# Kernel tuning notes

Measured on AMD Instinct MI355X. Metric: run time of the kernel, lower is better.

## Reference

```python
import jax, jax.numpy as jnp
import numpy as np

N = 10000
DIM = 64
F_CONST = 1.0
B_CONST = 0.1
R_CONST = 0.01


def setup_inputs() -> dict:
    key = jax.random.key(0)
    k1, k2 = jax.random.split(key)
    t = jnp.zeros((1,), dtype=jnp.float32)  # autonomous system; t unused
    x = jax.random.uniform(k1, (N, DIM), dtype=jnp.float32)
    A = jax.random.uniform(k2, (N, N), dtype=jnp.float32)
    return {"t": t, "x": x, "A": A}


def reference(t, x, A):
    # dx/dt = f - b*x - diag(A @ (r * x x^T)).reshape(-1, 1)
    # diag(A @ x x^T)_i = sum_j A_ij <x_j, x_i> = <x_i, (A @ x)_i>
    # so the interaction term is r * rowsum(x * (A @ x)) -- same math, no NxN intermediate.
    Ax = A @ x                                        # [N, DIM]
    outer = R_CONST * jnp.sum(x * Ax, axis=1, keepdims=True)  # [N, 1]
    return F_CONST - B_CONST * x - outer              # [N, DIM] via broadcast
```

## Files before the change

### kernel.cpp

```cpp
#include <hip/hip_runtime.h>
#include <stdint.h>


#define N_ROWS 10000
#define DIM 64
#define KTILE 32
#define NKT 320
#define CHUNK_K 256
#define CHUNKS_PER_Y 20
#define F_CONST 1.0f
#define B_CONST 0.1f
#define R_CONST 0.01f

#define SACC_OFF_BYTES 1310720

typedef __attribute__((ext_vector_type(8))) short s16x8;
typedef __attribute__((ext_vector_type(4))) float f32x4;
typedef __attribute__((ext_vector_type(4))) uint32_t u32x4;
typedef __attribute__((ext_vector_type(2))) uint32_t u32x2;

__device__ __forceinline__ uint32_t pack_bf16(float a, float b) {
    uint32_t ua = __builtin_bit_cast(uint32_t, a);
    uint32_t ub = __builtin_bit_cast(uint32_t, b);
    ua += 0x7FFFu + ((ua >> 16) & 1u);
    ub += 0x7FFFu + ((ub >> 16) & 1u);
    return (ua >> 16) | (ub & 0xFFFF0000u);
}

__global__ __launch_bounds__(256) void pack_x_kernel(const float* __restrict__ x,
                                                     uint32_t* __restrict__ ws,
                                                     float* __restrict__ sacc) {
    int id = blockIdx.x * 256 + threadIdx.x;
    if (id < N_ROWS) sacc[id] = 0.0f;
    int frag = id >> 6;
    int L = id & 63;
    int t = frag >> 2;
    int c = frag & 3;
    int k0 = t * KTILE + (L >> 4) * 8;
    int col = c * 16 + (L & 15);
    float v[8];
#pragma unroll
    for (int j = 0; j < 8; ++j) {
        int k = k0 + j;
        v[j] = (k < N_ROWS) ? x[k * DIM + col] : 0.0f;
    }
    u32x4 p;
    p.x = pack_bf16(v[0], v[1]);
    p.y = pack_bf16(v[2], v[3]);
    p.z = pack_bf16(v[4], v[5]);
    p.w = pack_bf16(v[6], v[7]);
    ((u32x4*)ws)[id] = p;
}

__global__ __launch_bounds__(256, 4) void gemm_dot_kernel(
    const float* __restrict__ A, const float* __restrict__ x,
    const uint32_t* __restrict__ ws, float* __restrict__ sacc) {
    __shared__ __align__(16) unsigned short lds[2][16 * CHUNK_K];

    int tid = threadIdx.x;
    int w = tid >> 6;
    int L = tid & 63;
    int quad = L >> 4;
    int m = L & 15;
    int rbase = blockIdx.x * 16;
    int c0 = blockIdx.y * CHUNKS_PER_Y;
    int c1 = c0 + CHUNKS_PER_Y;
    const float* Ab = A + (size_t)rbase * N_ROWS;

    f32x4 acc[4] = {{0.f, 0.f, 0.f, 0.f},
                    {0.f, 0.f, 0.f, 0.f},
                    {0.f, 0.f, 0.f, 0.f},
                    {0.f, 0.f, 0.f, 0.f}};

    {
        f32x4 ld[4];
#pragma unroll
        for (int i = 0; i < 4; ++i) {
            int row = i * 4 + w;
            int kg = c0 * CHUNK_K + L * 4;
            int ks = (kg <= N_ROWS - 4) ? kg : (N_ROWS - 4);
            ld[i] = __builtin_nontemporal_load((const f32x4*)(Ab + (size_t)row * N_ROWS + ks));
        }
#pragma unroll
        for (int i = 0; i < 4; ++i) {
            int row = i * 4 + w;
            int unit = (L >> 1) ^ (row & 7);
            u32x2 pk;
            pk.x = pack_bf16(ld[i].x, ld[i].y);
            pk.y = pack_bf16(ld[i].z, ld[i].w);
            *(u32x2*)((char*)lds[0] + row * 512 + (unit << 4) + ((L & 1) << 3)) = pk;
        }
    }
    __syncthreads();

    int p = 0;
    for (int c = c0; c < c1; ++c) {
        f32x4 ld[4];
        bool more = (c + 1 < c1);
        if (more) {
#pragma unroll
            for (int i = 0; i < 4; ++i) {
                int row = i * 4 + w;
                int kg = (c + 1) * CHUNK_K + L * 4;
                int ks = (kg <= N_ROWS - 4) ? kg : (N_ROWS - 4);
                ld[i] = __builtin_nontemporal_load((const f32x4*)(Ab + (size_t)row * N_ROWS + ks));
            }
        }

#pragma unroll
        for (int u = 0; u < 2; ++u) {
            int tt = w + 4 * u;
            int T = c * 8 + tt;
            int unit = (tt * 4 + quad) ^ (m & 7);
            s16x8 afrag = *(const s16x8*)((const char*)lds[p] + m * 512 + (unit << 4));
            const u32x4* pb = (const u32x4*)ws + (size_t)T * 256 + L;
#pragma unroll
            for (int cc = 0; cc < 4; ++cc) {
                s16x8 bfrag = __builtin_bit_cast(s16x8, pb[cc * 64]);
                acc[cc] = __builtin_amdgcn_mfma_f32_16x16x32_bf16(afrag, bfrag, acc[cc], 0, 0, 0);
            }
        }

        if (more) {
#pragma unroll
            for (int i = 0; i < 4; ++i) {
                int row = i * 4 + w;
                int unit = (L >> 1) ^ (row & 7);
                u32x2 pk;
                pk.x = pack_bf16(ld[i].x, ld[i].y);
                pk.y = pack_bf16(ld[i].z, ld[i].w);
                *(u32x2*)((char*)lds[p ^ 1] + row * 512 + (unit << 4) + ((L & 1) << 3)) = pk;
            }
        }
        __syncthreads();
        p ^= 1;
    }

    float pr[4];
#pragma unroll
    for (int r = 0; r < 4; ++r) {
        int grow = rbase + quad * 4 + r;
        const float* xr = x + (size_t)grow * DIM + m;
        pr[r] = acc[0][r] * xr[0] + acc[1][r] * xr[16] +
                acc[2][r] * xr[32] + acc[3][r] * xr[48];
        pr[r] += __shfl_xor(pr[r], 1);
        pr[r] += __shfl_xor(pr[r], 2);
        pr[r] += __shfl_xor(pr[r], 4);
        pr[r] += __shfl_xor(pr[r], 8);
    }
    if (m == 0) {
#pragma unroll
        for (int r = 0; r < 4; ++r)
            atomicAdd(&sacc[rbase + quad * 4 + r], pr[r]);
    }
}

__global__ __launch_bounds__(256) void finalize_kernel(const float* __restrict__ x,
                                                       const float* __restrict__ sacc,
                                                       float* __restrict__ out) {
    int id = blockIdx.x * 256 + threadIdx.x;
    f32x4 xv = ((const f32x4*)x)[id];
    float s = R_CONST * sacc[id >> 4];
    f32x4 o;
    o.x = F_CONST - B_CONST * xv.x - s;
    o.y = F_CONST - B_CONST * xv.y - s;
    o.z = F_CONST - B_CONST * xv.z - s;
    o.w = F_CONST - B_CONST * xv.w - s;
    ((f32x4*)out)[id] = o;
}

extern "C" void kernel_launch(void* const* d_in, const int* in_sizes, int n_in,
                              void* d_out, int out_size, void* d_ws, size_t ws_size,
                              hipStream_t stream) {
    const float* x = (const float*)d_in[1];
    const float* A = (const float*)d_in[2];
    float* out = (float*)d_out;
    uint32_t* ws = (uint32_t*)d_ws;
    float* sacc = (float*)((char*)d_ws + SACC_OFF_BYTES);

    pack_x_kernel<<<320, 256, 0, stream>>>(x, ws, sacc);
    gemm_dot_kernel<<<dim3(625, 2), 256, 0, stream>>>(A, x, ws, sacc);
    finalize_kernel<<<625, 256, 0, stream>>>(x, sacc, out);
}
```

Measured before the change: 523.9 us.

## Load A fragments straight into registers, drop LDS staging and barriers

The GEMM kernel no longer stages A tiles through double-buffered shared memory with block-wide barriers. Each wave now loads its A fragments directly from global memory in MFMA operand layout, converts them to bf16 in registers, and works through its own contiguous range of 40 K tiles. A-tile loads are prefetched four tiles ahead and packed-x tiles two ahead. This removes LDS writes and reads and the per-chunk `__syncthreads`. In exchange, each row is now read in 128-byte segments rather than long contiguous runs, register pressure is higher, and each wave issues its own atomic adds.

```diff
diff --git a/kernel.cpp b/kernel.cpp
--- a/kernel.cpp
+++ b/kernel.cpp
@@ -6,8 +6,9 @@
 #define DIM 64
 #define KTILE 32
 #define NKT 320
-#define CHUNK_K 256
-#define CHUNKS_PER_Y 20
+#define KSPLIT 2
+#define TPW 40
+#define PF 4
 #define F_CONST 1.0f
 #define B_CONST 0.1f
 #define R_CONST 0.01f
@@ -17,7 +18,6 @@
 typedef __attribute__((ext_vector_type(8))) short s16x8;
 typedef __attribute__((ext_vector_type(4))) float f32x4;
 typedef __attribute__((ext_vector_type(4))) uint32_t u32x4;
-typedef __attribute__((ext_vector_type(2))) uint32_t u32x2;
 
 __device__ __forceinline__ uint32_t pack_bf16(float a, float b) {
     uint32_t ua = __builtin_bit_cast(uint32_t, a);
@@ -25,6 +25,15 @@
     ua += 0x7FFFu + ((ua >> 16) & 1u);
     ub += 0x7FFFu + ((ub >> 16) & 1u);
     return (ua >> 16) | (ub & 0xFFFF0000u);
+}
+
+__device__ __forceinline__ s16x8 pack_frag(f32x4 lo, f32x4 hi) {
+    u32x4 p;
+    p.x = pack_bf16(lo.x, lo.y);
+    p.y = pack_bf16(lo.z, lo.w);
+    p.z = pack_bf16(hi.x, hi.y);
+    p.w = pack_bf16(hi.z, hi.w);
+    return __builtin_bit_cast(s16x8, p);
 }
 
 __global__ __launch_bounds__(256) void pack_x_kernel(const float* __restrict__ x,
@@ -55,85 +64,59 @@
 __global__ __launch_bounds__(256, 4) void gemm_dot_kernel(
     const float* __restrict__ A, const float* __restrict__ x,
     const uint32_t* __restrict__ ws, float* __restrict__ sacc) {
-    __shared__ __align__(16) unsigned short lds[2][16 * CHUNK_K];
-
     int tid = threadIdx.x;
     int w = tid >> 6;
     int L = tid & 63;
     int quad = L >> 4;
     int m = L & 15;
     int rbase = blockIdx.x * 16;
-    int c0 = blockIdx.y * CHUNKS_PER_Y;
-    int c1 = c0 + CHUNKS_PER_Y;
-    const float* Ab = A + (size_t)rbase * N_ROWS;
+    int t0 = (blockIdx.y * 4 + w) * TPW;
+
+    const float* Ar = A + (size_t)(rbase + m) * N_ROWS;
+    const u32x4* pb = (const u32x4*)ws;
+
+    auto aload = [&](int t, f32x4& lo, f32x4& hi) {
+        int k = t * KTILE + quad * 8;
+        if (k > N_ROWS - 8) k = N_ROWS - 8;
+        lo = __builtin_nontemporal_load((const f32x4*)(Ar + k));
+        hi = __builtin_nontemporal_load((const f32x4*)(Ar + k + 4));
+    };
+    auto bload = [&](int t, int cc) -> u32x4 {
+        return pb[(size_t)t * 256 + cc * 64 + L];
+    };
 
     f32x4 acc[4] = {{0.f, 0.f, 0.f, 0.f},
                     {0.f, 0.f, 0.f, 0.f},
                     {0.f, 0.f, 0.f, 0.f},
                     {0.f, 0.f, 0.f, 0.f}};
 
-    {
-        f32x4 ld[4];
-#pragma unroll
-        for (int i = 0; i < 4; ++i) {
-            int row = i * 4 + w;
-            int kg = c0 * CHUNK_K + L * 4;
-            int ks = (kg <= N_ROWS - 4) ? kg : (N_ROWS - 4);
-            ld[i] = __builtin_nontemporal_load((const f32x4*)(Ab + (size_t)row * N_ROWS + ks));
-        }
-#pragma unroll
-        for (int i = 0; i < 4; ++i) {
-            int row = i * 4 + w;
-            int unit = (L >> 1) ^ (row & 7);
-            u32x2 pk;
-            pk.x = pack_bf16(ld[i].x, ld[i].y);
-            pk.y = pack_bf16(ld[i].z, ld[i].w);
-            *(u32x2*)((char*)lds[0] + row * 512 + (unit << 4) + ((L & 1) << 3)) = pk;
-        }
-    }
-    __syncthreads();
-
-    int p = 0;
-    for (int c = c0; c < c1; ++c) {
-        f32x4 ld[4];
-        bool more = (c + 1 < c1);
-        if (more) {
-#pragma unroll
-            for (int i = 0; i < 4; ++i) {
-                int row = i * 4 + w;
-                int kg = (c + 1) * CHUNK_K + L * 4;
-                int ks = (kg <= N_ROWS - 4) ? kg : (N_ROWS - 4);
-                ld[i] = __builtin_nontemporal_load((const f32x4*)(Ab + (size_t)row * N_ROWS + ks));
-            }
-        }
+    f32x4 alo[PF], ahi[PF];
+    u32x4 bb[2][4];
 
 #pragma unroll
-        for (int u = 0; u < 2; ++u) {
-            int tt = w + 4 * u;
-            int T = c * 8 + tt;
-            int unit = (tt * 4 + quad) ^ (m & 7);
-            s16x8 afrag = *(const s16x8*)((const char*)lds[p] + m * 512 + (unit << 4));
-            const u32x4* pb = (const u32x4*)ws + (size_t)T * 256 + L;
+    for (int u = 0; u < PF; ++u) aload(t0 + u, alo[u], ahi[u]);
 #pragma unroll
-            for (int cc = 0; cc < 4; ++cc) {
-                s16x8 bfrag = __builtin_bit_cast(s16x8, pb[cc * 64]);
-                acc[cc] = __builtin_amdgcn_mfma_f32_16x16x32_bf16(afrag, bfrag, acc[cc], 0, 0, 0);
+    for (int cc = 0; cc < 4; ++cc) bb[0][cc] = bload(t0, cc);
+#pragma unroll
+    for (int cc = 0; cc < 4; ++cc) bb[1][cc] = bload(t0 + 1, cc);
+
+    for (int tb = 0; tb < TPW; tb += PF) {
+#pragma unroll
+        for (int u = 0; u < PF; ++u) {
+            int i = tb + u;
+            int t = t0 + i;
+            s16x8 af = pack_frag(alo[u], ahi[u]);
+#pragma unroll
+            for (int cc = 0; cc < 4; ++cc)
+                acc[cc] = __builtin_amdgcn_mfma_f32_16x16x32_bf16(
+                    af, __builtin_bit_cast(s16x8, bb[u & 1][cc]), acc[cc], 0, 0, 0);
+            if (i + 2 < TPW) {
+#pragma unroll
+                for (int cc = 0; cc < 4; ++cc) bb[u & 1][cc] = bload(t + 2, cc);
             }
+            if (i + PF < TPW)
+                aload(t + PF, alo[u], ahi[u]);
         }
-
-        if (more) {
-#pragma unroll
-            for (int i = 0; i < 4; ++i) {
-                int row = i * 4 + w;
-                int unit = (L >> 1) ^ (row & 7);
-                u32x2 pk;
-                pk.x = pack_bf16(ld[i].x, ld[i].y);
-                pk.y = pack_bf16(ld[i].z, ld[i].w);
-                *(u32x2*)((char*)lds[p ^ 1] + row * 512 + (unit << 4) + ((L & 1) << 3)) = pk;
-            }
-        }
-        __syncthreads();
-        p ^= 1;
     }
 
     float pr[4];
@@ -179,6 +162,6 @@
     float* sacc = (float*)((char*)d_ws + SACC_OFF_BYTES);
 
     pack_x_kernel<<<320, 256, 0, stream>>>(x, ws, sacc);
-    gemm_dot_kernel<<<dim3(625, 2), 256, 0, stream>>>(A, x, ws, sacc);
+    gemm_dot_kernel<<<dim3(625, KSPLIT), 256, 0, stream>>>(A, x, ws, sacc);
     finalize_kernel<<<625, 256, 0, stream>>>(x, sacc, out);
 }
```

After: 587.3 us. +12.1%, slower.
